# Kernel optimization log

Hardware: AMD Instinct MI355X
Metric: run time of the kernel (lower is better)

The kernel has to match this reference:

```python
import jax, jax.numpy as jnp
import numpy as np

R = 0.15          # ball-query radius (module init arg r)
K = 32            # _MAX_NEIGHBOURS
B, N = 8, 4096


def _ball_query(pos, r, k):
    """Dense ball query. pos: [B,N,3] -> neighbor idx [B,N,K], sorted by distance.
    Slots with fewer than k in-radius neighbors are filled with the query's own
    index (self is always the first neighbor at distance 0), so their
    contribution to (f_i - f_j)^2 is exactly 0 -- matching torch-points-kernels'
    fill-with-first-neighbor behaviour."""
    d2 = jnp.sum((pos[:, :, None, :] - pos[:, None, :, :]) ** 2, axis=-1)  # [B,N,N]
    masked = jnp.where(d2 <= r * r, d2, jnp.inf)
    neg_vals, idx = jax.lax.top_k(-masked, k)          # ascending distance
    valid = neg_vals > -jnp.inf
    self_idx = jnp.arange(pos.shape[1])[None, :, None]
    return jnp.where(valid, idx, self_idx)             # [B,N,K]


def setup_inputs() -> dict:
    key = jax.random.key(0)
    k1, k2 = jax.random.split(key)
    pos = jax.random.uniform(k1, (B, N, 3), dtype=jnp.float32)
    f = jax.random.normal(k2, (B, N), dtype=jnp.float32)
    return {"pos": pos, "f": f}


def reference(pos, f):
    # neighbor indices are non-differentiable (torch gathers with long indices)
    nei_idx = jax.lax.stop_gradient(_ball_query(pos, R, K))      # [B,N,K]
    f_nei = jax.vmap(lambda fb, ib: fb[ib])(f, nei_idx)          # [B,N,K]
    variances = jnp.sum((f[:, :, None] - f_nei) ** 2, axis=-1)   # [B,N]
    return 0.5 * jnp.mean(variances)
```

## Files before the change

kernel.cpp:

```cpp
#include <hip/hip_runtime.h>


#define BQ_K 32
#define CAP 128
#define WPB 4
#define G 6
#define NC (G * G * G)
#define CMAX 64
#define CAPC 512
#define QMAX 64
#define NPTS 4096

__device__ __forceinline__ int cell_coord(float x) {
    int c = (int)(x * (float)G);
    return c < 0 ? 0 : (c > G - 1 ? G - 1 : c);
}

__device__ __forceinline__ unsigned int decode_cnt(unsigned int v) {
    return (v >= 0x80000000u) ? (v - 0xAAAAAAAAu) : v;
}

__device__ __forceinline__ float select_sum(float2 e0, float2 e1, int M,
                                            float r2) {
    if (M <= BQ_K) return e0.y + e1.y;
    float lo = 0.0f, hi = r2 * 1.000001f;
    #pragma unroll
    for (int it = 0; it < 12; ++it) {
        const float mid = 0.5f * (lo + hi);
        const int cnt = __popcll(__ballot(e0.x < mid)) +
                        __popcll(__ballot(e1.x < mid));
        if (cnt >= BQ_K) hi = mid; else lo = mid;
    }
    float s = 0.0f;
    if (e0.x < hi) s = e0.y;
    if (e1.x < hi) s += e1.y;
    return s;
}

__global__ void dl_scatter(const float* __restrict__ pos,
                           const float* __restrict__ f,
                           unsigned int* __restrict__ cnt,
                           float4* __restrict__ buck,
                           float* __restrict__ out, int total) {
    const int t = blockIdx.x * 256 + threadIdx.x;
    if (t == 0) out[0] = 0.0f;
    if (t >= total) return;
    const int b = t >> 12;
    const float x = pos[3 * (size_t)t + 0];
    const float y = pos[3 * (size_t)t + 1];
    const float z = pos[3 * (size_t)t + 2];
    const int c = (cell_coord(z) * G + cell_coord(y)) * G + cell_coord(x);
    const int cell = b * NC + c;
    const unsigned int old = atomicAdd(&cnt[cell], 1u);
    const unsigned int slot = decode_cnt(old);
    if (slot < CMAX)
        buck[(size_t)cell * CMAX + slot] = make_float4(x, y, z, f[t]);
}

__global__ __launch_bounds__(256) void dl_main(
    const unsigned int* __restrict__ cnt, const float4* __restrict__ buck,
    float* __restrict__ out, float r2, float scale)
{
    __shared__ float4 s_cand[CAPC];
    __shared__ float2 s_sel[WPB][CAP];
    __shared__ int    s_q[QMAX];
    __shared__ int    s_ncand, s_nq;
    __shared__ float  s_wsum[WPB];
    __shared__ int    s_cell[27];
    __shared__ int    s_cc[27];

    const int bc = blockIdx.x;
    const int b  = bc / NC;
    const int c  = bc - b * NC;
    const int cx = c % G, cy = (c / G) % G, cz = c / (G * G);

    const int lane = threadIdx.x & 63;
    const int wave = threadIdx.x >> 6;
    const unsigned long long lmask = (1ULL << lane) - 1ULL;

    if (threadIdx.x == 0) { s_ncand = 0; s_nq = 0; }
    if (threadIdx.x < 27) {
        const int n = threadIdx.x;
        const int nx = cx + (n % 3) - 1;
        const int ny = cy + ((n / 3) % 3) - 1;
        const int nz = cz + (n / 9) - 1;
        int cell = -1;
        unsigned int cc = 0;
        if ((unsigned)nx < (unsigned)G && (unsigned)ny < (unsigned)G &&
            (unsigned)nz < (unsigned)G) {
            cell = b * NC + (nz * G + ny) * G + nx;
            cc = decode_cnt(cnt[cell]);
            cc = cc < CMAX ? cc : CMAX;
        }
        s_cell[n] = cell;
        s_cc[n]   = (int)cc;
    }
    __syncthreads();

    const float lox = cx * (1.0f / G), hix = lox + (1.0f / G);
    const float loy = cy * (1.0f / G), hiy = loy + (1.0f / G);
    const float loz = cz * (1.0f / G), hiz = loz + (1.0f / G);

    for (int n = wave; n < 27; n += WPB) {
        const int cc = s_cc[n];
        if (cc == 0) continue;
        const int cell = s_cell[n];
        const float4 p = buck[(size_t)cell * CMAX + lane];
        const bool have = lane < cc;
        const float ddx = fmaxf(fmaxf(lox - p.x, p.x - hix), 0.0f);
        const float ddy = fmaxf(fmaxf(loy - p.y, p.y - hiy), 0.0f);
        const float ddz = fmaxf(fmaxf(loz - p.z, p.z - hiz), 0.0f);
        const float d2c = fmaf(ddx, ddx, fmaf(ddy, ddy, ddz * ddz));
        const bool in = have && (d2c <= r2);
        const unsigned long long m = __ballot(in);
        const int nh = __popcll(m);
        int base = 0;
        if (lane == 0 && nh) base = atomicAdd(&s_ncand, nh);
        base = __shfl(base, 0, 64);
        if (in) {
            const int off = base + __popcll(m & lmask);
            if (off < CAPC) {
                s_cand[off] = p;
                if (n == 13) {
                    const int qs = atomicAdd(&s_nq, 1);
                    if (qs < QMAX) s_q[qs] = off;
                }
            }
        }
    }
    __syncthreads();

    const int ncand = s_ncand < CAPC ? s_ncand : CAPC;
    const int nq    = s_nq < QMAX ? s_nq : QMAX;
    const int ncB   = (ncand + 63) & ~63;

    float2* sel = s_sel[wave];
    float wsum = 0.0f;

    for (int qi = wave; qi < nq; qi += WPB) {
        const float4 qp = s_cand[s_q[qi]];
        const float qx = qp.x, qy = qp.y, qz = qp.z, fi = qp.w;

        int cin = 0;
        for (int basej = 0; basej < ncB; basej += 64) {
            const float4 cd = s_cand[basej + lane];
            const bool valid = (basej + lane) < ncand;
            const float dx = cd.x - qx, dy = cd.y - qy, dz = cd.z - qz;
            const float d2 = fmaf(dx, dx, fmaf(dy, dy, dz * dz));
            const bool inb = valid && (d2 <= r2);
            const unsigned long long mm = __ballot(inb);
            const int off = cin + __popcll(mm & lmask);
            if (inb && off < CAP) {
                const float fd = fi - cd.w;
                sel[off] = make_float2(d2, fd * fd);
            }
            cin += __popcll(mm);
        }
        const int M = cin < CAP ? cin : CAP;

        const float2 e0 = (lane < M) ? sel[lane]
                                     : make_float2(1e30f, 0.0f);
        const float2 e1 = (64 + lane < M) ? sel[64 + lane]
                                          : make_float2(1e30f, 0.0f);
        wsum += select_sum(e0, e1, M, r2);
    }

    for (int o = 32; o > 0; o >>= 1) wsum += __shfl_down(wsum, o, 64);
    if (lane == 0) s_wsum[wave] = wsum;
    __syncthreads();
    if (threadIdx.x == 0) {
        const float bs = s_wsum[0] + s_wsum[1] + s_wsum[2] + s_wsum[3];
        atomicAdd(out, bs * scale);
    }
}

__global__ __launch_bounds__(256) void dl_fallback(
    const float* __restrict__ pos, const float* __restrict__ f,
    float* __restrict__ out, float r2, float scale)
{
    __shared__ float4 s_cand[CAPC];
    __shared__ float2 s_sel[WPB][CAP];
    __shared__ int    s_q[QMAX];
    __shared__ int    s_ncand, s_nq;
    __shared__ float  s_wsum[WPB];

    const int bc = blockIdx.x;
    const int b  = bc / NC;
    const int c  = bc - b * NC;
    const int cx = c % G, cy = (c / G) % G, cz = c / (G * G);
    const int lane = threadIdx.x & 63;
    const int wave = threadIdx.x >> 6;
    const unsigned long long lmask = (1ULL << lane) - 1ULL;

    if (threadIdx.x == 0) { s_ncand = 0; s_nq = 0; }
    __syncthreads();

    const float* posb = pos + (size_t)b * NPTS * 3;
    const float* fb   = f   + (size_t)b * NPTS;
    const float lox = cx * (1.0f / G), hix = lox + (1.0f / G);
    const float loy = cy * (1.0f / G), hiy = loy + (1.0f / G);
    const float loz = cz * (1.0f / G), hiz = loz + (1.0f / G);

    constexpr int per = NPTS / WPB;
    const int wbeg = wave * per;
    for (int j0 = 0; j0 < per; j0 += 64) {
        const int j = wbeg + j0 + lane;
        const float x  = posb[3 * j + 0];
        const float y  = posb[3 * j + 1];
        const float z  = posb[3 * j + 2];
        const float ddx = fmaxf(fmaxf(lox - x, x - hix), 0.0f);
        const float ddy = fmaxf(fmaxf(loy - y, y - hiy), 0.0f);
        const float ddz = fmaxf(fmaxf(loz - z, z - hiz), 0.0f);
        const float d2c = fmaf(ddx, ddx, fmaf(ddy, ddy, ddz * ddz));
        const bool in = (d2c <= r2);
        const unsigned long long m = __ballot(in);
        const int nh = __popcll(m);
        int base = 0;
        if (lane == 0 && nh) base = atomicAdd(&s_ncand, nh);
        base = __shfl(base, 0, 64);
        if (in) {
            const int off = base + __popcll(m & lmask);
            if (off < CAPC) {
                s_cand[off] = make_float4(x, y, z, fb[j]);
                if (cell_coord(x) == cx && cell_coord(y) == cy &&
                    cell_coord(z) == cz) {
                    const int qs = atomicAdd(&s_nq, 1);
                    if (qs < QMAX) s_q[qs] = off;
                }
            }
        }
    }
    __syncthreads();

    const int ncand = s_ncand < CAPC ? s_ncand : CAPC;
    const int nq    = s_nq < QMAX ? s_nq : QMAX;
    const int ncB   = (ncand + 63) & ~63;
    float2* sel = s_sel[wave];
    float wsum = 0.0f;

    for (int qi = wave; qi < nq; qi += WPB) {
        const float4 qp = s_cand[s_q[qi]];
        const float qx = qp.x, qy = qp.y, qz = qp.z, fi = qp.w;
        int cin = 0;
        for (int basej = 0; basej < ncB; basej += 64) {
            const float4 cd = s_cand[basej + lane];
            const bool valid = (basej + lane) < ncand;
            const float dx = cd.x - qx, dy = cd.y - qy, dz = cd.z - qz;
            const float d2 = fmaf(dx, dx, fmaf(dy, dy, dz * dz));
            const bool inb = valid && (d2 <= r2);
            const unsigned long long mm = __ballot(inb);
            const int off = cin + __popcll(mm & lmask);
            if (inb && off < CAP) {
                const float fd = fi - cd.w;
                sel[off] = make_float2(d2, fd * fd);
            }
            cin += __popcll(mm);
        }
        const int M = cin < CAP ? cin : CAP;
        const float2 e0 = (lane < M) ? sel[lane] : make_float2(1e30f, 0.0f);
        const float2 e1 = (64 + lane < M) ? sel[64 + lane]
                                          : make_float2(1e30f, 0.0f);
        wsum += select_sum(e0, e1, M, r2);
    }

    for (int o = 32; o > 0; o >>= 1) wsum += __shfl_down(wsum, o, 64);
    if (lane == 0) s_wsum[wave] = wsum;
    __syncthreads();
    if (threadIdx.x == 0) {
        const float bs = s_wsum[0] + s_wsum[1] + s_wsum[2] + s_wsum[3];
        atomicAdd(out, bs * scale);
    }
}

extern "C" void kernel_launch(void* const* d_in, const int* in_sizes, int n_in,
                              void* d_out, int out_size, void* d_ws, size_t ws_size,
                              hipStream_t stream) {
    const float* pos = (const float*)d_in[0];
    const float* f   = (const float*)d_in[1];
    float* out = (float*)d_out;

    const int B = in_sizes[1] / NPTS;
    const int total = B * NPTS;
    const float r2 = 0.15f * 0.15f;
    const float scale = 0.5f / (float)total;

    const size_t cnt_bytes  = (size_t)B * NC * sizeof(int);
    const size_t buck_bytes = (size_t)B * NC * CMAX * sizeof(float4);
    if (ws_size < cnt_bytes + buck_bytes) {
        hipMemsetAsync(out, 0, sizeof(float), stream);
        dl_fallback<<<B * NC, 256, 0, stream>>>(pos, f, out, r2, scale);
        return;
    }

    unsigned int* cnt  = (unsigned int*)d_ws;
    float4*       buck = (float4*)((char*)d_ws + cnt_bytes);

    dl_scatter<<<(total + 255) / 256, 256, 0, stream>>>(pos, f, cnt, buck,
                                                        out, total);
    dl_main   <<<B * NC, 256, 0, stream>>>(cnt, buck, out, r2, scale);
}
```

Measured before the change: 89.34 us.

## Software-pipeline bisection selection of previous query into next query's distance scan

Defers the top-K bisection for each query and interleaves its steps, two per 64-candidate chunk, into the next query's distance-scan loop. The goal is to hide ballot and popcount latency behind shared-memory loads. It also pads the candidate array to a multiple of 64 with far-away sentinels, which removes the per-lane validity check, and skips the second ballot when M is 64 or less. In exchange it keeps more registers live and adds branching inside the inner loop.

Measured after the change: 89.04 us. Within noise of the previous version (-0.3%).

```diff
diff --git a/kernel.cpp b/kernel.cpp
--- a/kernel.cpp
+++ b/kernel.cpp
@@ -18,6 +18,14 @@
 
 __device__ __forceinline__ unsigned int decode_cnt(unsigned int v) {
     return (v >= 0x80000000u) ? (v - 0xAAAAAAAAu) : v;
+}
+
+__device__ __forceinline__ void bis_step(const float2& e0, const float2& e1,
+                                         bool big, float& lo, float& hi) {
+    const float mid = 0.5f * (lo + hi);
+    int cnt = __popcll(__ballot(e0.x < mid));
+    if (big) cnt += __popcll(__ballot(e1.x < mid));
+    if (cnt >= BQ_K) hi = mid; else lo = mid;
 }
 
 __device__ __forceinline__ float select_sum(float2 e0, float2 e1, int M,
@@ -134,8 +142,17 @@
     const int nq    = s_nq < QMAX ? s_nq : QMAX;
     const int ncB   = (ncand + 63) & ~63;
 
+    for (int i = ncand + threadIdx.x; i < ncB; i += 256)
+        s_cand[i] = make_float4(1e30f, 1e30f, 1e30f, 0.0f);
+    __syncthreads();
+
     float2* sel = s_sel[wave];
     float wsum = 0.0f;
+
+    float2 pe0 = make_float2(1e30f, 0.0f), pe1 = make_float2(1e30f, 0.0f);
+    float plo = 0.0f, phi = 1e31f;
+    int   prem = 0;
+    bool  pneed = false, pbig = false, phave = false;
 
     for (int qi = wave; qi < nq; qi += WPB) {
         const float4 qp = s_cand[s_q[qi]];
@@ -144,10 +161,13 @@
         int cin = 0;
         for (int basej = 0; basej < ncB; basej += 64) {
             const float4 cd = s_cand[basej + lane];
-            const bool valid = (basej + lane) < ncand;
+            if (pneed && prem > 0) {
+                bis_step(pe0, pe1, pbig, plo, phi); --prem;
+                if (prem > 0) { bis_step(pe0, pe1, pbig, plo, phi); --prem; }
+            }
             const float dx = cd.x - qx, dy = cd.y - qy, dz = cd.z - qz;
             const float d2 = fmaf(dx, dx, fmaf(dy, dy, dz * dz));
-            const bool inb = valid && (d2 <= r2);
+            const bool inb = d2 <= r2;
             const unsigned long long mm = __ballot(inb);
             const int off = cin + __popcll(mm & lmask);
             if (inb && off < CAP) {
@@ -156,13 +176,34 @@
             }
             cin += __popcll(mm);
         }
+        if (pneed) {
+            while (prem > 0) { bis_step(pe0, pe1, pbig, plo, phi); --prem; }
+        }
+        if (phave) {
+            float s = 0.0f;
+            if (pe0.x < phi) s = pe0.y;
+            if (pe1.x < phi) s += pe1.y;
+            wsum += s;
+        }
         const int M = cin < CAP ? cin : CAP;
-
-        const float2 e0 = (lane < M) ? sel[lane]
-                                     : make_float2(1e30f, 0.0f);
-        const float2 e1 = (64 + lane < M) ? sel[64 + lane]
-                                          : make_float2(1e30f, 0.0f);
-        wsum += select_sum(e0, e1, M, r2);
+        pe0 = (lane < M) ? sel[lane] : make_float2(1e30f, 0.0f);
+        pe1 = (64 + lane < M) ? sel[64 + lane] : make_float2(1e30f, 0.0f);
+        phave = true;
+        pneed = (M > BQ_K);
+        pbig  = (M > 64);
+        plo   = 0.0f;
+        phi   = pneed ? r2 * 1.000001f : 1e31f;
+        prem  = 12;
+    }
+    if (pneed) {
+        #pragma unroll
+        for (int it = 0; it < 12; ++it) bis_step(pe0, pe1, pbig, plo, phi);
+    }
+    if (phave) {
+        float s = 0.0f;
+        if (pe0.x < phi) s = pe0.y;
+        if (pe1.x < phi) s += pe1.y;
+        wsum += s;
     }
 
     for (int o = 32; o > 0; o >>= 1) wsum += __shfl_down(wsum, o, 64);
```
